# Performance work log

Hardware: AMD Instinct MI355X
Metric: run time of the kernel (lower is better)

## Reference

```python
import jax, jax.numpy as jnp
import numpy as np


def setup_inputs() -> dict:
    key = jax.random.key(0)
    k1, k2, k3, k4 = jax.random.split(key, 4)
    B, D, N, M = 4, 256, 4096, 4096
    return {
        "src": jax.random.normal(k1, (B, 3, N), dtype=jnp.float32),
        "tgt": jax.random.normal(k2, (B, 3, M), dtype=jnp.float32),
        "src_emb": jax.random.normal(k3, (B, D, N), dtype=jnp.float32),
        "tgt_emb": jax.random.normal(k4, (B, D, M), dtype=jnp.float32),
    }


def reference(src, tgt, src_emb, tgt_emb):
    # pairwise_distance[b,n,m] = -||src_emb[:,n] - tgt_emb[:,m]||^2
    # decomposed as -xx + 2*inner - yy (inner below is -2*dot, as in torch code)
    inner = -2.0 * jnp.einsum("bdn,bdm->bnm", src_emb, tgt_emb)       # [B,N,M]
    xx = jnp.sum(src_emb ** 2, axis=1)[:, :, None]                     # [B,N,1]
    yy = jnp.sum(tgt_emb ** 2, axis=1)[:, None, :]                     # [B,1,M]
    pairwise_distance = -xx - inner - yy                               # [B,N,M]
    scores = jax.nn.softmax(pairwise_distance, axis=2)                 # softmax over tgt points
    # src_corr[b,c,n] = sum_m tgt[b,c,m] * scores[b,n,m]
    src_corr = jnp.einsum("bcm,bnm->bcn", tgt, scores)                 # [B,3,N]
    return src_corr
```

## Files before the change

### kernel.cpp

```cpp
#include <hip/hip_runtime.h>

#define NBATCH 4
#define DDIM   256
#define NN     4096
#define MM     4096
#define NCHUNK 8
#define MCHUNK 512
#define MTILE  32
#define LOG2E  1.44269504088896340736f

using half8  = __attribute__((ext_vector_type(8))) _Float16;
using floatx4 = __attribute__((ext_vector_type(4))) float;

__global__ __launch_bounds__(256) void k_transpose(const float* __restrict__ src_emb,
                                                   const float* __restrict__ tgt_emb,
                                                   _Float16* __restrict__ Qh,
                                                   _Float16* __restrict__ Kh) {
    __shared__ float tile[64][65];
    int bz = blockIdx.z;
    int tensor = bz >> 2, b = bz & 3;
    const float* in = tensor ? tgt_emb : src_emb;
    _Float16* out   = tensor ? Kh : Qh;
    int n0 = blockIdx.x * 64, d0 = blockIdx.y * 64;
    int t = threadIdx.x;
    int c = t & 63, r0 = t >> 6;
    const float* ip = in + (size_t)(b * DDIM + d0) * NN + n0 + c;
#pragma unroll
    for (int i = 0; i < 16; i++) {
        int r = r0 + i * 4;
        tile[r][c] = ip[(size_t)r * NN];
    }
    __syncthreads();
    _Float16* op = out + (size_t)(b * NN + n0) * DDIM + d0 + c;
#pragma unroll
    for (int i = 0; i < 16; i++) {
        int r = r0 + i * 4;
        op[(size_t)r * DDIM] = (_Float16)tile[c][r];
    }
}

__global__ __launch_bounds__(256) void k_yyvt(const float* __restrict__ tgt,
                                              const float* __restrict__ tgt_emb,
                                              float* __restrict__ yy,
                                              float4* __restrict__ Vt) {
    int b = blockIdx.y;
    int m = blockIdx.x * 256 + threadIdx.x;
    const float* p = tgt_emb + (size_t)b * DDIM * MM + m;
    float s = 0.f;
#pragma unroll 8
    for (int d = 0; d < DDIM; d++) { float v = p[(size_t)d * MM]; s = fmaf(v, v, s); }
    yy[b * MM + m] = s * (-LOG2E);
    const float* tp = tgt + (size_t)b * 3 * MM + m;
    Vt[b * MM + m] = make_float4(tp[0], tp[MM], tp[2 * MM], 1.0f);
}

__global__ __launch_bounds__(256, 2) void k_flash(const _Float16* __restrict__ Qh,
                                                  const _Float16* __restrict__ Kh,
                                                  const float* __restrict__ yy,
                                                  const float4* __restrict__ Vt,
                                                  float4* __restrict__ Opart,
                                                  float* __restrict__ Mpart) {
    __shared__ half8   Kt8[MTILE * 33];
    __shared__ floatx4 yyt4[MTILE / 4];
    __shared__ float4  vtt[MTILE];

    int i = blockIdx.x;
    int xcd = i & 7, s = i >> 3;
    int grp = xcd + 8 * (s >> 4);
    int b = grp >> 3, chunk = grp & 7, ntile = s & 15;

    int t = threadIdx.x, wave = t >> 6, lane = t & 63, quad = lane >> 4, l15 = lane & 15;
    int n0 = ntile * 256 + wave * 64;

    const half8* qp = (const half8*)Qh + (size_t)b * NN * 32;
    half8 qf[4][8];
#pragma unroll
    for (int nb = 0; nb < 4; nb++) {
        int n = n0 + nb * 16 + l15;
#pragma unroll
        for (int ds = 0; ds < 8; ds++) qf[nb][ds] = qp[n * 32 + ds * 4 + quad];
    }

    const floatx4 z4 = {0.f, 0.f, 0.f, 0.f};
    floatx4 o[4] = {z4, z4, z4, z4};
    float mr[4] = {-__builtin_inff(), -__builtin_inff(), -__builtin_inff(), -__builtin_inff()};

    const half8* kp = (const half8*)Kh + (size_t)b * MM * 32;
    int m0 = chunk * MCHUNK;
    int srow = t >> 5, sdc = t & 31;

    for (int mt = 0; mt < MCHUNK / MTILE; mt++) {
        int mg = m0 + mt * MTILE;
        __syncthreads();
#pragma unroll
        for (int it = 0; it < 4; it++) {
            int mrow = srow + it * 8;
            Kt8[mrow * 33 + sdc] = kp[(size_t)(mg + mrow) * 32 + sdc];
        }
        if (t < MTILE / 4) yyt4[t] = ((const floatx4*)(yy + b * MM + mg))[t];
        else if (t >= 64 && t < 64 + MTILE) vtt[t - 64] = Vt[b * MM + mg + (t - 64)];
        __syncthreads();

        floatx4 acc[4][2];
#pragma unroll
        for (int nb = 0; nb < 4; nb++) { acc[nb][0] = z4; acc[nb][1] = z4; }
#pragma unroll
        for (int ds = 0; ds < 8; ds++) {
            half8 a0 = Kt8[l15 * 33 + ds * 4 + quad];
            half8 a1 = Kt8[(16 + l15) * 33 + ds * 4 + quad];
#pragma unroll
            for (int nb = 0; nb < 4; nb++) {
                acc[nb][0] = __builtin_amdgcn_mfma_f32_16x16x32_f16(a0, qf[nb][ds], acc[nb][0], 0, 0, 0);
                acc[nb][1] = __builtin_amdgcn_mfma_f32_16x16x32_f16(a1, qf[nb][ds], acc[nb][1], 0, 0, 0);
            }
        }

        floatx4 yv0 = yyt4[quad], yv1 = yyt4[4 + quad];
#pragma unroll
        for (int nb = 0; nb < 4; nb++) {
            float sv[8];
#pragma unroll
            for (int r = 0; r < 4; r++) {
                sv[r]     = fmaf(acc[nb][0][r], 2.f * LOG2E, yv0[r]);
                sv[4 + r] = fmaf(acc[nb][1][r], 2.f * LOG2E, yv1[r]);
            }
            float tm = sv[0];
#pragma unroll
            for (int r = 1; r < 8; r++) tm = fmaxf(tm, sv[r]);
            tm = fmaxf(tm, __shfl_xor(tm, 16, 64));
            tm = fmaxf(tm, __shfl_xor(tm, 32, 64));
            float mnew  = fmaxf(mr[nb], tm);
            float alpha = __builtin_amdgcn_exp2f(mr[nb] - mnew);
            mr[nb] = mnew;
            floatx4 oa = o[nb] * alpha;
#pragma unroll
            for (int mb = 0; mb < 2; mb++) {
#pragma unroll
                for (int r = 0; r < 4; r++) {
                    float p = __builtin_amdgcn_exp2f(sv[mb * 4 + r] - mnew);
                    float4 v = vtt[mb * 16 + quad * 4 + r];
                    oa[0] = fmaf(p, v.x, oa[0]);
                    oa[1] = fmaf(p, v.y, oa[1]);
                    oa[2] = fmaf(p, v.z, oa[2]);
                    oa[3] = fmaf(p, v.w, oa[3]);
                }
            }
            o[nb] = oa;
        }
    }

#pragma unroll
    for (int nb = 0; nb < 4; nb++) {
#pragma unroll
        for (int c = 0; c < 4; c++) {
            float v = o[nb][c];
            v += __shfl_xor(v, 16, 64);
            v += __shfl_xor(v, 32, 64);
            o[nb][c] = v;
        }
    }
    if (quad == 0) {
#pragma unroll
        for (int nb = 0; nb < 4; nb++) {
            int n = n0 + nb * 16 + l15;
            size_t idx = (size_t)(chunk * NBATCH + b) * NN + n;
            Opart[idx] = make_float4(o[nb][0], o[nb][1], o[nb][2], o[nb][3]);
            Mpart[idx] = mr[nb];
        }
    }
}

__global__ __launch_bounds__(256) void k_combine(const float4* __restrict__ Opart,
                                                 const float* __restrict__ Mpart,
                                                 float* __restrict__ out) {
    int idx = blockIdx.x * 256 + threadIdx.x;
    int b = idx >> 12, n = idx & (NN - 1);
    float mstar = -__builtin_inff();
#pragma unroll
    for (int j = 0; j < NCHUNK; j++)
        mstar = fmaxf(mstar, Mpart[(size_t)(j * NBATCH + b) * NN + n]);
    float o0 = 0.f, o1 = 0.f, o2 = 0.f, l = 0.f;
#pragma unroll
    for (int j = 0; j < NCHUNK; j++) {
        size_t id = (size_t)(j * NBATCH + b) * NN + n;
        float w = __builtin_amdgcn_exp2f(Mpart[id] - mstar);
        float4 P = Opart[id];
        o0 = fmaf(w, P.x, o0); o1 = fmaf(w, P.y, o1);
        o2 = fmaf(w, P.z, o2); l  = fmaf(w, P.w, l);
    }
    out[(size_t)(b * 3 + 0) * NN + n] = o0 / l;
    out[(size_t)(b * 3 + 1) * NN + n] = o1 / l;
    out[(size_t)(b * 3 + 2) * NN + n] = o2 / l;
}

extern "C" void kernel_launch(void* const* d_in, const int* in_sizes, int n_in,
                              void* d_out, int out_size, void* d_ws, size_t ws_size,
                              hipStream_t stream) {
    const float* tgt     = (const float*)d_in[1];
    const float* src_emb = (const float*)d_in[2];
    const float* tgt_emb = (const float*)d_in[3];
    float* out = (float*)d_out;

    char* ws = (char*)d_ws;
    _Float16* Qh   = (_Float16*)(ws);
    _Float16* Kh   = (_Float16*)(ws + 8388608);
    float*    yy   = (float*)   (ws + 16777216);
    float4*   Vt   = (float4*)  (ws + 16842752);
    float4*   Op   = (float4*)  (ws + 17104896);
    float*    Mp   = (float*)   (ws + 19202048);

    hipLaunchKernelGGL(k_transpose, dim3(64, 4, 8), dim3(256), 0, stream, src_emb, tgt_emb, Qh, Kh);
    hipLaunchKernelGGL(k_yyvt,      dim3(16, 4),    dim3(256), 0, stream, tgt, tgt_emb, yy, Vt);
    hipLaunchKernelGGL(k_flash,     dim3(512),      dim3(256), 0, stream, Qh, Kh, yy, Vt, Op, Mp);
    hipLaunchKernelGGL(k_combine,   dim3(64),       dim3(256), 0, stream, Op, Mp, out);
}
```

Measured before the change: 145.8 us.

## Widen flash M-tile, fold scale into Q, compute yy from fp16 K

Doubles the key tile to 64 rows so each wave issues 16 MFMAs per depth step, and reorganizes the softmax epilogue into vector max/subtract passes. The 2*log2e scale is folded into the fp16 Q conversion, and the transpose now writes 16-byte half8 stores instead of scalar halves. yy is recomputed from the already-transposed fp16 K with coalesced reads, and the separate Vt buffer is dropped in favor of reading tgt directly inside the flash kernel. This removes strided fp32 reads of tgt_emb and one workspace pass, at the cost of more accumulator registers (risking spills at 2 blocks per CU) and slightly lower yy precision from fp16 inputs.

Measured after the change: 141.5 us. 1.03x faster.

```diff
diff --git a/kernel.cpp b/kernel.cpp
--- a/kernel.cpp
+++ b/kernel.cpp
@@ -6,63 +6,72 @@
 #define MM     4096
 #define NCHUNK 8
 #define MCHUNK 512
-#define MTILE  32
+#define MTILE  64
 #define LOG2E  1.44269504088896340736f
 
-using half8  = __attribute__((ext_vector_type(8))) _Float16;
+using half8   = __attribute__((ext_vector_type(8))) _Float16;
 using floatx4 = __attribute__((ext_vector_type(4))) float;
 
-__global__ __launch_bounds__(256) void k_transpose(const float* __restrict__ src_emb,
-                                                   const float* __restrict__ tgt_emb,
-                                                   _Float16* __restrict__ Qh,
-                                                   _Float16* __restrict__ Kh) {
+__global__ __launch_bounds__(256) void k_prep(const float* __restrict__ src_emb,
+                                              const float* __restrict__ tgt_emb,
+                                              _Float16* __restrict__ Qh,
+                                              _Float16* __restrict__ Kh) {
     __shared__ float tile[64][65];
     int bz = blockIdx.z;
     int tensor = bz >> 2, b = bz & 3;
     const float* in = tensor ? tgt_emb : src_emb;
     _Float16* out   = tensor ? Kh : Qh;
+    const float scale = tensor ? 1.0f : 2.0f * LOG2E;
     int n0 = blockIdx.x * 64, d0 = blockIdx.y * 64;
     int t = threadIdx.x;
-    int c = t & 63, r0 = t >> 6;
-    const float* ip = in + (size_t)(b * DDIM + d0) * NN + n0 + c;
-#pragma unroll
-    for (int i = 0; i < 16; i++) {
-        int r = r0 + i * 4;
-        tile[r][c] = ip[(size_t)r * NN];
+    {
+        int c = t & 63, r0 = t >> 6;
+        const float* ip = in + (size_t)(b * DDIM + d0) * NN + n0 + c;
+#pragma unroll
+        for (int i = 0; i < 16; i++) {
+            int r = r0 + i * 4;
+            tile[r][c] = ip[(size_t)r * NN];
+        }
     }
     __syncthreads();
-    _Float16* op = out + (size_t)(b * NN + n0) * DDIM + d0 + c;
-#pragma unroll
-    for (int i = 0; i < 16; i++) {
-        int r = r0 + i * 4;
-        op[(size_t)r * DDIM] = (_Float16)tile[c][r];
-    }
-}
-
-__global__ __launch_bounds__(256) void k_yyvt(const float* __restrict__ tgt,
-                                              const float* __restrict__ tgt_emb,
-                                              float* __restrict__ yy,
-                                              float4* __restrict__ Vt) {
+    int dg = t & 7, nn = t >> 3;
+#pragma unroll
+    for (int pass = 0; pass < 2; pass++) {
+        int n = nn + pass * 32;
+        half8 h;
+#pragma unroll
+        for (int k = 0; k < 8; k++) h[k] = (_Float16)(tile[dg * 8 + k][n] * scale);
+        *(half8*)(out + (size_t)(b * NN + n0 + n) * DDIM + d0 + dg * 8) = h;
+    }
+}
+
+__global__ __launch_bounds__(256) void k_yy(const _Float16* __restrict__ Kh,
+                                            float* __restrict__ yy) {
     int b = blockIdx.y;
-    int m = blockIdx.x * 256 + threadIdx.x;
-    const float* p = tgt_emb + (size_t)b * DDIM * MM + m;
+    int m = blockIdx.x * 64 + (threadIdx.x >> 2);
+    int j = threadIdx.x & 3;
+    const half8* p = (const half8*)(Kh + (size_t)(b * MM + m) * DDIM);
     float s = 0.f;
-#pragma unroll 8
-    for (int d = 0; d < DDIM; d++) { float v = p[(size_t)d * MM]; s = fmaf(v, v, s); }
-    yy[b * MM + m] = s * (-LOG2E);
-    const float* tp = tgt + (size_t)b * 3 * MM + m;
-    Vt[b * MM + m] = make_float4(tp[0], tp[MM], tp[2 * MM], 1.0f);
+#pragma unroll
+    for (int k = 0; k < 8; k++) {
+        half8 v = p[k * 4 + j];
+#pragma unroll
+        for (int e = 0; e < 8; e++) { float f = (float)v[e]; s = fmaf(f, f, s); }
+    }
+    s += __shfl_xor(s, 1, 64);
+    s += __shfl_xor(s, 2, 64);
+    if (j == 0) yy[b * MM + m] = s * (-LOG2E);
 }
 
 __global__ __launch_bounds__(256, 2) void k_flash(const _Float16* __restrict__ Qh,
                                                   const _Float16* __restrict__ Kh,
                                                   const float* __restrict__ yy,
-                                                  const float4* __restrict__ Vt,
+                                                  const float* __restrict__ tgt,
                                                   float4* __restrict__ Opart,
                                                   float* __restrict__ Mpart) {
     __shared__ half8   Kt8[MTILE * 33];
     __shared__ floatx4 yyt4[MTILE / 4];
-    __shared__ float4  vtt[MTILE];
+    __shared__ floatx4 vtt[MTILE];
 
     int i = blockIdx.x;
     int xcd = i & 7, s = i >> 3;
@@ -86,6 +95,7 @@
     float mr[4] = {-__builtin_inff(), -__builtin_inff(), -__builtin_inff(), -__builtin_inff()};
 
     const half8* kp = (const half8*)Kh + (size_t)b * MM * 32;
+    const float* tb = tgt + (size_t)b * 3 * MM;
     int m0 = chunk * MCHUNK;
     int srow = t >> 5, sdc = t & 31;
 
@@ -93,59 +103,70 @@
         int mg = m0 + mt * MTILE;
         __syncthreads();
 #pragma unroll
-        for (int it = 0; it < 4; it++) {
+        for (int it = 0; it < 8; it++) {
             int mrow = srow + it * 8;
             Kt8[mrow * 33 + sdc] = kp[(size_t)(mg + mrow) * 32 + sdc];
         }
-        if (t < MTILE / 4) yyt4[t] = ((const floatx4*)(yy + b * MM + mg))[t];
-        else if (t >= 64 && t < 64 + MTILE) vtt[t - 64] = Vt[b * MM + mg + (t - 64)];
+        if (t < MTILE) {
+            int m = mg + t;
+            floatx4 v = {tb[m], tb[MM + m], tb[2 * MM + m], 1.0f};
+            vtt[t] = v;
+        } else if (t < MTILE + MTILE / 4) {
+            yyt4[t - MTILE] = ((const floatx4*)(yy + b * MM + mg))[t - MTILE];
+        }
         __syncthreads();
 
-        floatx4 acc[4][2];
-#pragma unroll
-        for (int nb = 0; nb < 4; nb++) { acc[nb][0] = z4; acc[nb][1] = z4; }
+        floatx4 acc[4][4];
+#pragma unroll
+        for (int nb = 0; nb < 4; nb++)
+#pragma unroll
+            for (int mb = 0; mb < 4; mb++) acc[nb][mb] = z4;
 #pragma unroll
         for (int ds = 0; ds < 8; ds++) {
-            half8 a0 = Kt8[l15 * 33 + ds * 4 + quad];
-            half8 a1 = Kt8[(16 + l15) * 33 + ds * 4 + quad];
-#pragma unroll
-            for (int nb = 0; nb < 4; nb++) {
-                acc[nb][0] = __builtin_amdgcn_mfma_f32_16x16x32_f16(a0, qf[nb][ds], acc[nb][0], 0, 0, 0);
-                acc[nb][1] = __builtin_amdgcn_mfma_f32_16x16x32_f16(a1, qf[nb][ds], acc[nb][1], 0, 0, 0);
-            }
-        }
-
-        floatx4 yv0 = yyt4[quad], yv1 = yyt4[4 + quad];
+            half8 a[4];
+#pragma unroll
+            for (int mb = 0; mb < 4; mb++) a[mb] = Kt8[(mb * 16 + l15) * 33 + ds * 4 + quad];
+#pragma unroll
+            for (int nb = 0; nb < 4; nb++)
+#pragma unroll
+                for (int mb = 0; mb < 4; mb++)
+                    acc[nb][mb] = __builtin_amdgcn_mfma_f32_16x16x32_f16(a[mb], qf[nb][ds], acc[nb][mb], 0, 0, 0);
+        }
+
+#pragma unroll
+        for (int mb = 0; mb < 4; mb++) {
+            floatx4 yv = yyt4[mb * 4 + quad];
+#pragma unroll
+            for (int nb = 0; nb < 4; nb++) acc[nb][mb] = acc[nb][mb] + yv;
+        }
 #pragma unroll
         for (int nb = 0; nb < 4; nb++) {
-            float sv[8];
-#pragma unroll
-            for (int r = 0; r < 4; r++) {
-                sv[r]     = fmaf(acc[nb][0][r], 2.f * LOG2E, yv0[r]);
-                sv[4 + r] = fmaf(acc[nb][1][r], 2.f * LOG2E, yv1[r]);
-            }
-            float tm = sv[0];
-#pragma unroll
-            for (int r = 1; r < 8; r++) tm = fmaxf(tm, sv[r]);
+            floatx4 mx = __builtin_elementwise_max(
+                __builtin_elementwise_max(acc[nb][0], acc[nb][1]),
+                __builtin_elementwise_max(acc[nb][2], acc[nb][3]));
+            float tm = fmaxf(fmaxf(mx[0], mx[1]), fmaxf(mx[2], mx[3]));
             tm = fmaxf(tm, __shfl_xor(tm, 16, 64));
             tm = fmaxf(tm, __shfl_xor(tm, 32, 64));
-            float mnew  = fmaxf(mr[nb], tm);
-            float alpha = __builtin_amdgcn_exp2f(mr[nb] - mnew);
-            mr[nb] = mnew;
-            floatx4 oa = o[nb] * alpha;
-#pragma unroll
-            for (int mb = 0; mb < 2; mb++) {
+            float mn = fmaxf(mr[nb], tm);
+            float al = __builtin_amdgcn_exp2f(mr[nb] - mn);
+            mr[nb] = mn;
+            o[nb] = o[nb] * al;
+            floatx4 mnv = {mn, mn, mn, mn};
+#pragma unroll
+            for (int mb = 0; mb < 4; mb++) acc[nb][mb] = acc[nb][mb] - mnv;
+        }
+#pragma unroll
+        for (int mb = 0; mb < 4; mb++) {
+            floatx4 vr[4];
+#pragma unroll
+            for (int r = 0; r < 4; r++) vr[r] = vtt[mb * 16 + quad * 4 + r];
+#pragma unroll
+            for (int nb = 0; nb < 4; nb++)
 #pragma unroll
                 for (int r = 0; r < 4; r++) {
-                    float p = __builtin_amdgcn_exp2f(sv[mb * 4 + r] - mnew);
-                    float4 v = vtt[mb * 16 + quad * 4 + r];
-                    oa[0] = fmaf(p, v.x, oa[0]);
-                    oa[1] = fmaf(p, v.y, oa[1]);
-                    oa[2] = fmaf(p, v.z, oa[2]);
-                    oa[3] = fmaf(p, v.w, oa[3]);
+                    float p = __builtin_amdgcn_exp2f(acc[nb][mb][r]);
+                    o[nb] = o[nb] + p * vr[r];
                 }
-            }
-            o[nb] = oa;
         }
     }
 
@@ -202,15 +223,14 @@
     float* out = (float*)d_out;
 
     char* ws = (char*)d_ws;
-    _Float16* Qh   = (_Float16*)(ws);
-    _Float16* Kh   = (_Float16*)(ws + 8388608);
-    float*    yy   = (float*)   (ws + 16777216);
-    float4*   Vt   = (float4*)  (ws + 16842752);
-    float4*   Op   = (float4*)  (ws + 17104896);
-    float*    Mp   = (float*)   (ws + 19202048);
-
-    hipLaunchKernelGGL(k_transpose, dim3(64, 4, 8), dim3(256), 0, stream, src_emb, tgt_emb, Qh, Kh);
-    hipLaunchKernelGGL(k_yyvt,      dim3(16, 4),    dim3(256), 0, stream, tgt, tgt_emb, yy, Vt);
-    hipLaunchKernelGGL(k_flash,     dim3(512),      dim3(256), 0, stream, Qh, Kh, yy, Vt, Op, Mp);
-    hipLaunchKernelGGL(k_combine,   dim3(64),       dim3(256), 0, stream, Op, Mp, out);
-}
+    _Float16* Qh = (_Float16*)(ws);
+    _Float16* Kh = (_Float16*)(ws + 8388608);
+    float*    yy = (float*)   (ws + 16777216);
+    float4*   Op = (float4*)  (ws + 16842752);
+    float*    Mp = (float*)   (ws + 18939904);
+
+    hipLaunchKernelGGL(k_prep,    dim3(64, 4, 8), dim3(256), 0, stream, src_emb, tgt_emb, Qh, Kh);
+    hipLaunchKernelGGL(k_yy,      dim3(64, 4),    dim3(256), 0, stream, Kh, yy);
+    hipLaunchKernelGGL(k_flash,   dim3(512),      dim3(256), 0, stream, Qh, Kh, yy, tgt, Op, Mp);
+    hipLaunchKernelGGL(k_combine, dim3(64),       dim3(256), 0, stream, Op, Mp, out);
+}
```
